# Kernel tuning notes

Measured on AMD Instinct MI355X. Metric: run time of the kernel, lower is better.

Reference implementation:

```python
import jax, jax.numpy as jnp
import numpy as np

N_NODES = 100000

def sage_conv(x, edge_index, Wl, bl, Wr):
    # PyG SAGEConv, aggr='add', normalize=False:
    #   out = lin_l(sum_{j in N(i)} x_j) + lin_r(x_i)
    src, dst = edge_index[0], edge_index[1]
    agg = jax.ops.segment_sum(x[src], dst, num_segments=N_NODES)  # [N, F]
    return agg @ Wl.T + bl + x @ Wr.T


def setup_inputs() -> dict:
    key = jax.random.key(0)
    ks = jax.random.split(key, 7)
    F_IN, HID, C, E = 128, 256, 50, 640000
    x = jax.random.normal(ks[0], (N_NODES, F_IN), dtype=jnp.float32)
    edge_index = jax.random.randint(ks[1], (2, E), 0, N_NODES, dtype=jnp.int64)
    s1 = 1.0 / np.sqrt(F_IN)
    s2 = 1.0 / np.sqrt(HID)
    return {
        "x": x,
        "edge_index": edge_index,
        "W1l": jax.random.normal(ks[2], (HID, F_IN), dtype=jnp.float32) * s1,
        "b1l": jnp.zeros((HID,), dtype=jnp.float32),
        "W1r": jax.random.normal(ks[3], (HID, F_IN), dtype=jnp.float32) * s1,
        "W2l": jax.random.normal(ks[4], (C, HID), dtype=jnp.float32) * s2,
        "b2l": jnp.zeros((C,), dtype=jnp.float32),
        "W2r": jax.random.normal(ks[5], (C, HID), dtype=jnp.float32) * s2,
    }


def reference(x, edge_index, W1l, b1l, W1r, W2l, b2l, W2r):
    h = sage_conv(x, edge_index, W1l, b1l, W1r)
    h = jax.nn.relu(h)
    # F.dropout(p=0.5, training=False) is identity in eval mode
    out = sage_conv(h, edge_index, W2l, b2l, W2r)
    return out
```

## Files before the change

kernel.cpp:

```cpp
#include <hip/hip_runtime.h>

#define N_NODES 100000
#define MPAD    100096
#define F_IN 128
#define HID 256
#define C_OUT 50
#define N_EDGES 640000
#define CAP 32
#define NRANGE 391
#define P1BLK 256
#define EPB (N_EDGES / P1BLK)
#define CCAP 32
#define XBLK 12500

typedef __attribute__((ext_vector_type(8))) short short8;
typedef __attribute__((ext_vector_type(8))) ushort us8;
typedef __attribute__((ext_vector_type(4))) float f32x4;

struct alignas(8) us4 { ushort x, y, z, w; };

__device__ __forceinline__ ushort f2bf(float f) {
    union { float f; unsigned u; } v; v.f = f;
    unsigned r = (v.u + 0x7fffu + ((v.u >> 16) & 1u)) >> 16;
    return (ushort)r;
}

__device__ __forceinline__ float bf2f(ushort u) {
    union { unsigned u; float f; } v; v.u = ((unsigned)u) << 16;
    return v.f;
}

__device__ __forceinline__ void load_lds16(const void* gsrc, void* lds) {
    __builtin_amdgcn_global_load_lds(
        (const __attribute__((address_space(1))) void*)gsrc,
        (__attribute__((address_space(3))) void*)lds, 16, 0, 0);
}

__global__ void prep_kernel(const float* __restrict__ W1l, const float* __restrict__ W1r,
                            const float* __restrict__ W2l, const float* __restrict__ W2r,
                            ushort* __restrict__ B1t, ushort* __restrict__ B2t) {
    int idx = blockIdx.x * blockDim.x + threadIdx.x;
    if (idx < 256 * 256) {
        int o = idx >> 8, k = idx & 255;
        float v = (k < 128) ? W1l[o * 128 + k] : W1r[o * 128 + (k - 128)];
        B1t[o * 256 + k] = f2bf(v);
    }
    if (idx < 128 * 256) {
        int c = idx >> 8, k = idx & 255;
        float v = 0.f;
        if (c < C_OUT) v = W2l[c * 256 + k];
        else if (c >= 64 && c < 64 + C_OUT) v = W2r[(c - 64) * 256 + k];
        B2t[c * 256 + k] = f2bf(v);
    }
}

__global__ __launch_bounds__(256) void phase1_xcvt(const int* __restrict__ src,
                                                   const int* __restrict__ dst,
                                                   int* __restrict__ cnt1,
                                                   int* __restrict__ subbucket,
                                                   const float* __restrict__ x,
                                                   ushort* __restrict__ A1) {
    __shared__ int lcnt[NRANGE];
    int b = blockIdx.x;
    if (b < P1BLK) {
        for (int r = threadIdx.x; r < NRANGE; r += 256) lcnt[r] = 0;
        __syncthreads();
        int base = b * EPB;
        for (int i = base + (int)threadIdx.x; i < base + EPB; i += 256) {
            int d = dst[i];
            int s = src[i];
            int r = d >> 8;
            int p = atomicAdd(&lcnt[r], 1);
            if (p < CCAP) subbucket[((size_t)r * P1BLK + b) * CCAP + p] = ((d & 255) << 24) | s;
        }
        __syncthreads();
        for (int r = threadIdx.x; r < NRANGE; r += 256) cnt1[r * P1BLK + b] = lcnt[r];
    } else {
        int tid = (b - P1BLK) * 256 + threadIdx.x;
        int node = tid >> 5, q = tid & 31;
        if (node >= N_NODES) return;
        float4 v = *reinterpret_cast<const float4*>(x + (size_t)node * F_IN + q * 4);
        us4 o;
        o.x = f2bf(v.x); o.y = f2bf(v.y); o.z = f2bf(v.z); o.w = f2bf(v.w);
        *reinterpret_cast<us4*>(&A1[(size_t)node * 256 + 128 + q * 4]) = o;
    }
}

__global__ __launch_bounds__(256) void phase2_merge(const int* __restrict__ cnt1,
                                                    const int* __restrict__ subbucket,
                                                    int* __restrict__ cnt,
                                                    int* __restrict__ bucket) {
    __shared__ int lcnt2[256];
    __shared__ int lbuf[256 * CAP];
    int r = blockIdx.x, t = threadIdx.x;
    lcnt2[t] = 0;
    __syncthreads();
    int n = cnt1[r * P1BLK + t];
    if (n > CCAP) n = CCAP;
    size_t cbase = ((size_t)r * P1BLK + t) * CCAP;
    for (int k = 0; k < n; ++k) {
        unsigned u = (unsigned)subbucket[cbase + k];
        int dl = u >> 24;
        int p = atomicAdd(&lcnt2[dl], 1);
        if (p < CAP) lbuf[dl * CAP + p] = (int)(u & 0xFFFFFF);
    }
    __syncthreads();
    int node0 = r << 8;
    if (node0 + t < N_NODES) cnt[node0 + t] = lcnt2[t];
    for (int idx = t; idx < 256 * CAP; idx += 256) {
        if (node0 + (idx >> 5) < N_NODES) bucket[(size_t)node0 * CAP + idx] = lbuf[idx];
    }
}

__global__ void gather1_kernel(const int* __restrict__ cnt, const int* __restrict__ bucket,
                               ushort* __restrict__ A1) {
    int tid = blockIdx.x * blockDim.x + threadIdx.x;
    int node = tid >> 4, q = tid & 15;
    if (node >= N_NODES) return;
    int n = cnt[node];
    if (n > CAP) n = CAP;
    const int* row = bucket + (size_t)node * CAP;
    float a[8];
#pragma unroll
    for (int j = 0; j < 8; ++j) a[j] = 0.f;
    int p = 0;
    while (p + 8 <= n) {
        us8 v[8];
#pragma unroll
        for (int t = 0; t < 8; ++t) {
            int s = row[p + t];
            v[t] = *reinterpret_cast<const us8*>(&A1[(size_t)s * 256 + 128 + q * 8]);
        }
#pragma unroll
        for (int t = 0; t < 8; ++t)
#pragma unroll
            for (int j = 0; j < 8; ++j) a[j] += bf2f(v[t][j]);
        p += 8;
    }
    int rem = n - p;
    if (rem > 0) {
        us8 v[7];
#pragma unroll
        for (int t = 0; t < 7; ++t) {
            int s = (t < rem) ? row[p + t] : row[p];
            v[t] = *reinterpret_cast<const us8*>(&A1[(size_t)s * 256 + 128 + q * 8]);
        }
#pragma unroll
        for (int t = 0; t < 7; ++t) {
            if (t < rem) {
#pragma unroll
                for (int j = 0; j < 8; ++j) a[j] += bf2f(v[t][j]);
            }
        }
    }
    us8 o;
#pragma unroll
    for (int j = 0; j < 8; ++j) o[j] = f2bf(a[j]);
    *reinterpret_cast<us8*>(&A1[(size_t)node * 256 + q * 8]) = o;
}

__global__ void gather2_kernel(const ushort* __restrict__ g, const int* __restrict__ cnt,
                               const int* __restrict__ bucket, float* __restrict__ out) {
    int tid = blockIdx.x * blockDim.x + threadIdx.x;
    int node = tid >> 3, q = tid & 7;
    if (node >= N_NODES) return;
    int c = q * 8;
    if (c >= C_OUT) return;
    int n = cnt[node];
    if (n > CAP) n = CAP;
    const int* row = bucket + (size_t)node * CAP;
    float a[8];
#pragma unroll
    for (int j = 0; j < 8; ++j) a[j] = 0.f;
    int p = 0;
    while (p + 8 <= n) {
        us8 v[8];
#pragma unroll
        for (int t = 0; t < 8; ++t) {
            int s = row[p + t];
            v[t] = *reinterpret_cast<const us8*>(&g[(size_t)s * 64 + c]);
        }
#pragma unroll
        for (int t = 0; t < 8; ++t)
#pragma unroll
            for (int j = 0; j < 8; ++j) a[j] += bf2f(v[t][j]);
        p += 8;
    }
    int rem = n - p;
    if (rem > 0) {
        us8 v[7];
#pragma unroll
        for (int t = 0; t < 7; ++t) {
            int s = (t < rem) ? row[p + t] : row[p];
            v[t] = *reinterpret_cast<const us8*>(&g[(size_t)s * 64 + c]);
        }
#pragma unroll
        for (int t = 0; t < 7; ++t) {
            if (t < rem) {
#pragma unroll
                for (int j = 0; j < 8; ++j) a[j] += bf2f(v[t][j]);
            }
        }
    }
    float* po = out + (size_t)node * C_OUT;
#pragma unroll
    for (int j = 0; j < 8; ++j) {
        if (c + j < C_OUT) po[c + j] += a[j];
    }
}

__global__ __launch_bounds__(512) void gemm_fused(
    const ushort* __restrict__ A, const ushort* __restrict__ B1,
    const ushort* __restrict__ B2, const float* __restrict__ b1,
    const float* __restrict__ b2, ushort* __restrict__ gOut,
    float* __restrict__ oOut) {
    __shared__ alignas(16) ushort smem[36864];
    ushort* As  = smem;
    ushort* Bs  = smem + 4096;
    ushort* hL  = smem;
    ushort* Bs2 = smem + 32768;

    const int tid = threadIdx.x;
    const int lane = tid & 63, wid = tid >> 6;
    const int wr = wid >> 2, wc = wid & 3;
    const int brow = blockIdx.x;
    const int aoffA = (lane & 15) * 32 + (lane >> 4) * 8;

    f32x4 acc[4][4];
#pragma unroll
    for (int m = 0; m < 4; ++m)
#pragma unroll
        for (int n = 0; n < 4; ++n) acc[m][n] = (f32x4){0.f, 0.f, 0.f, 0.f};

    const int rA = tid >> 2, kA = (tid & 3) * 8;
    const int cB1 = tid + 512;
    const int rB1 = cB1 >> 2, kB1 = (cB1 & 3) * 8;
    const size_t aRow = (size_t)(brow * 128 + rA) * 256;

    for (int kt = 0; kt < 8; ++kt) {
        const int kOff = kt * 32;
        load_lds16(A + aRow + kOff + kA, &As[tid * 8]);
        load_lds16(B1 + (size_t)rA * 256 + kOff + kA, &Bs[tid * 8]);
        load_lds16(B1 + (size_t)rB1 * 256 + kOff + kB1, &Bs[cB1 * 8]);
        __syncthreads();

        short8 af[4], bfr[4];
#pragma unroll
        for (int m = 0; m < 4; ++m)
            af[m] = *reinterpret_cast<const short8*>(&As[(wr * 64 + m * 16) * 32 + aoffA]);
#pragma unroll
        for (int n = 0; n < 4; ++n)
            bfr[n] = *reinterpret_cast<const short8*>(&Bs[(wc * 64 + n * 16) * 32 + aoffA]);
#pragma unroll
        for (int m = 0; m < 4; ++m)
#pragma unroll
            for (int n = 0; n < 4; ++n)
                acc[m][n] = __builtin_amdgcn_mfma_f32_16x16x32_bf16(af[m], bfr[n], acc[m][n], 0, 0, 0);
        __syncthreads();
    }

    {
        const int colBase = wc * 64 + (lane & 15);
        const int lrBase = wr * 64 + ((lane >> 4) << 2);
        float bv[4];
#pragma unroll
        for (int n = 0; n < 4; ++n) bv[n] = b1[colBase + n * 16];
#pragma unroll
        for (int m = 0; m < 4; ++m) {
#pragma unroll
            for (int r = 0; r < 4; ++r) {
                int lr = lrBase + m * 16 + r;
#pragma unroll
                for (int n = 0; n < 4; ++n) {
                    float v = acc[m][n][r] + bv[n];
                    v = v > 0.f ? v : 0.f;
                    int ktc = wc * 2 + (n >> 1);
                    int kp = (n & 1) * 16 + (lane & 15);
                    hL[ktc * 4096 + lr * 32 + kp] = f2bf(v);
                }
            }
        }
    }
    __syncthreads();

    f32x4 acc2[4][2];
#pragma unroll
    for (int m = 0; m < 4; ++m)
#pragma unroll
        for (int n = 0; n < 2; ++n) acc2[m][n] = (f32x4){0.f, 0.f, 0.f, 0.f};

    for (int kt = 0; kt < 8; ++kt) {
        const int kOff = kt * 32;
        load_lds16(B2 + (size_t)rA * 256 + kOff + kA, &Bs2[tid * 8]);
        __syncthreads();

        short8 af[4], bfr[2];
#pragma unroll
        for (int m = 0; m < 4; ++m)
            af[m] = *reinterpret_cast<const short8*>(&hL[kt * 4096 + (wr * 64 + m * 16) * 32 + aoffA]);
#pragma unroll
        for (int n = 0; n < 2; ++n)
            bfr[n] = *reinterpret_cast<const short8*>(&Bs2[(wc * 32 + n * 16) * 32 + aoffA]);
#pragma unroll
        for (int m = 0; m < 4; ++m)
#pragma unroll
            for (int n = 0; n < 2; ++n)
                acc2[m][n] = __builtin_amdgcn_mfma_f32_16x16x32_bf16(af[m], bfr[n], acc2[m][n], 0, 0, 0);
        __syncthreads();
    }

    const int colB = wc * 32 + (lane & 15);
    const int rowB = brow * 128 + wr * 64 + ((lane >> 4) << 2);
#pragma unroll
    for (int m = 0; m < 4; ++m) {
#pragma unroll
        for (int r = 0; r < 4; ++r) {
            int row = rowB + m * 16 + r;
            if (row >= N_NODES) continue;
#pragma unroll
            for (int n = 0; n < 2; ++n) {
                int cg = colB + n * 16;
                float v = acc2[m][n][r];
                if (cg < 64) {
                    gOut[(size_t)row * 64 + cg] = f2bf(v);
                } else if (cg < 64 + C_OUT) {
                    oOut[(size_t)row * C_OUT + (cg - 64)] = v + b2[cg - 64];
                }
            }
        }
    }
}

extern "C" void kernel_launch(void* const* d_in, const int* in_sizes, int n_in,
                              void* d_out, int out_size, void* d_ws, size_t ws_size,
                              hipStream_t stream) {
    const float* x   = (const float*)d_in[0];
    const int*   ei  = (const int*)d_in[1];
    const float* W1l = (const float*)d_in[2];
    const float* b1l = (const float*)d_in[3];
    const float* W1r = (const float*)d_in[4];
    const float* W2l = (const float*)d_in[5];
    const float* b2l = (const float*)d_in[6];
    const float* W2r = (const float*)d_in[7];
    float* out = (float*)d_out;

    ushort* A1    = (ushort*)d_ws;
    ushort* B1t   = A1 + (size_t)MPAD * 256;
    ushort* B2t   = B1t + 256 * 256;
    ushort* g     = B2t + 128 * 256;
    int* cnt      = (int*)(g + (size_t)N_NODES * 64);
    int* bucket   = cnt + N_NODES;
    int* cnt1     = bucket + (size_t)N_NODES * CAP;
    int* subbucket= cnt1 + NRANGE * P1BLK;

    const int* src = ei;
    const int* dst = ei + N_EDGES;

    prep_kernel<<<256, 256, 0, stream>>>(W1l, W1r, W2l, W2r, B1t, B2t);
    phase1_xcvt<<<P1BLK + XBLK, 256, 0, stream>>>(src, dst, cnt1, subbucket, x, A1);
    phase2_merge<<<NRANGE, 256, 0, stream>>>(cnt1, subbucket, cnt, bucket);

    gather1_kernel<<<(N_NODES * 16 + 255) / 256, 256, 0, stream>>>(cnt, bucket, A1);

    const int nbrow = MPAD / 128;
    gemm_fused<<<nbrow, 512, 0, stream>>>(A1, B1t, B2t, b1l, b2l, g, out);

    gather2_kernel<<<(N_NODES * 8 + 255) / 256, 256, 0, stream>>>(g, cnt, bucket, out);
}
```

Baseline: 165.8 us.

## Split fused two-layer GEMM into separate kernels with hidden buffer in global memory

The fused kernel kept the hidden ReLU activations in LDS and ran the second GEMM in the same block. It is now split into two kernels. The first writes bf16 hidden activations to a new global workspace buffer, and the second reads them back and produces both g and the output. The split frees LDS in the first kernel, which may allow higher occupancy, but it adds roughly 51MB of global write and read traffic plus an extra launch.

```diff
diff --git a/kernel.cpp b/kernel.cpp
--- a/kernel.cpp
+++ b/kernel.cpp
@@ -209,39 +209,34 @@
     }
 }
 
-__global__ __launch_bounds__(512) void gemm_fused(
-    const ushort* __restrict__ A, const ushort* __restrict__ B1,
-    const ushort* __restrict__ B2, const float* __restrict__ b1,
-    const float* __restrict__ b2, ushort* __restrict__ gOut,
-    float* __restrict__ oOut) {
-    __shared__ alignas(16) ushort smem[36864];
-    ushort* As  = smem;
-    ushort* Bs  = smem + 4096;
-    ushort* hL  = smem;
-    ushort* Bs2 = smem + 32768;
-
+__global__ __launch_bounds__(512) void gemm1_512(
+    const ushort* __restrict__ A, const ushort* __restrict__ B,
+    const float* __restrict__ bias, ushort* __restrict__ hOut) {
+    __shared__ alignas(16) ushort As[128 * 32];
+    __shared__ alignas(16) ushort Bs[256 * 32];
     const int tid = threadIdx.x;
     const int lane = tid & 63, wid = tid >> 6;
     const int wr = wid >> 2, wc = wid & 3;
     const int brow = blockIdx.x;
+
+    f32x4 acc[4][4];
+#pragma unroll
+    for (int m = 0; m < 4; ++m)
+#pragma unroll
+        for (int n = 0; n < 4; ++n) acc[m][n] = (f32x4){0.f, 0.f, 0.f, 0.f};
+
+    const int rA = tid >> 2,          kA = (tid & 3) * 8;
+    const int cB1 = tid + 512;
+    const int rB1 = cB1 >> 2,         kB1 = (cB1 & 3) * 8;
+    const size_t aRow = (size_t)(brow * 128 + rA) * 256;
+
     const int aoffA = (lane & 15) * 32 + (lane >> 4) * 8;
-
-    f32x4 acc[4][4];
-#pragma unroll
-    for (int m = 0; m < 4; ++m)
-#pragma unroll
-        for (int n = 0; n < 4; ++n) acc[m][n] = (f32x4){0.f, 0.f, 0.f, 0.f};
-
-    const int rA = tid >> 2, kA = (tid & 3) * 8;
-    const int cB1 = tid + 512;
-    const int rB1 = cB1 >> 2, kB1 = (cB1 & 3) * 8;
-    const size_t aRow = (size_t)(brow * 128 + rA) * 256;
 
     for (int kt = 0; kt < 8; ++kt) {
         const int kOff = kt * 32;
         load_lds16(A + aRow + kOff + kA, &As[tid * 8]);
-        load_lds16(B1 + (size_t)rA * 256 + kOff + kA, &Bs[tid * 8]);
-        load_lds16(B1 + (size_t)rB1 * 256 + kOff + kB1, &Bs[cB1 * 8]);
+        load_lds16(B + (size_t)rA * 256 + kOff + kA, &Bs[tid * 8]);
+        load_lds16(B + (size_t)rB1 * 256 + kOff + kB1, &Bs[cB1 * 8]);
         __syncthreads();
 
         short8 af[4], bfr[4];
@@ -259,58 +254,12 @@
         __syncthreads();
     }
 
-    {
-        const int colBase = wc * 64 + (lane & 15);
-        const int lrBase = wr * 64 + ((lane >> 4) << 2);
-        float bv[4];
-#pragma unroll
-        for (int n = 0; n < 4; ++n) bv[n] = b1[colBase + n * 16];
-#pragma unroll
-        for (int m = 0; m < 4; ++m) {
-#pragma unroll
-            for (int r = 0; r < 4; ++r) {
-                int lr = lrBase + m * 16 + r;
-#pragma unroll
-                for (int n = 0; n < 4; ++n) {
-                    float v = acc[m][n][r] + bv[n];
-                    v = v > 0.f ? v : 0.f;
-                    int ktc = wc * 2 + (n >> 1);
-                    int kp = (n & 1) * 16 + (lane & 15);
-                    hL[ktc * 4096 + lr * 32 + kp] = f2bf(v);
-                }
-            }
-        }
-    }
-    __syncthreads();
-
-    f32x4 acc2[4][2];
-#pragma unroll
-    for (int m = 0; m < 4; ++m)
-#pragma unroll
-        for (int n = 0; n < 2; ++n) acc2[m][n] = (f32x4){0.f, 0.f, 0.f, 0.f};
-
-    for (int kt = 0; kt < 8; ++kt) {
-        const int kOff = kt * 32;
-        load_lds16(B2 + (size_t)rA * 256 + kOff + kA, &Bs2[tid * 8]);
-        __syncthreads();
-
-        short8 af[4], bfr[2];
-#pragma unroll
-        for (int m = 0; m < 4; ++m)
-            af[m] = *reinterpret_cast<const short8*>(&hL[kt * 4096 + (wr * 64 + m * 16) * 32 + aoffA]);
-#pragma unroll
-        for (int n = 0; n < 2; ++n)
-            bfr[n] = *reinterpret_cast<const short8*>(&Bs2[(wc * 32 + n * 16) * 32 + aoffA]);
-#pragma unroll
-        for (int m = 0; m < 4; ++m)
-#pragma unroll
-            for (int n = 0; n < 2; ++n)
-                acc2[m][n] = __builtin_amdgcn_mfma_f32_16x16x32_bf16(af[m], bfr[n], acc2[m][n], 0, 0, 0);
-        __syncthreads();
-    }
-
-    const int colB = wc * 32 + (lane & 15);
+    const int colB = wc * 64 + (lane & 15);
     const int rowB = brow * 128 + wr * 64 + ((lane >> 4) << 2);
+
+    float bv[4];
+#pragma unroll
+    for (int n = 0; n < 4; ++n) bv[n] = bias[colB + n * 16];
 #pragma unroll
     for (int m = 0; m < 4; ++m) {
 #pragma unroll
@@ -318,13 +267,82 @@
             int row = rowB + m * 16 + r;
             if (row >= N_NODES) continue;
 #pragma unroll
-            for (int n = 0; n < 2; ++n) {
+            for (int n = 0; n < 4; ++n) {
+                float v = acc[m][n][r] + bv[n];
+                v = v > 0.f ? v : 0.f;
+                hOut[(size_t)row * 256 + colB + n * 16] = f2bf(v);
+            }
+        }
+    }
+}
+
+__global__ __launch_bounds__(256) void gemm2_kernel(
+    const ushort* __restrict__ A, const ushort* __restrict__ B,
+    const float* __restrict__ bias, ushort* __restrict__ gOut,
+    float* __restrict__ oOut) {
+    __shared__ alignas(16) ushort As[128 * 32];
+    __shared__ alignas(16) ushort Bs[128 * 32];
+    const int tid = threadIdx.x;
+    const int lane = tid & 63, wid = tid >> 6;
+    const int wr = wid >> 1, wc = wid & 1;
+    const int brow = blockIdx.x;
+
+    f32x4 acc[4][4];
+#pragma unroll
+    for (int m = 0; m < 4; ++m)
+#pragma unroll
+        for (int n = 0; n < 4; ++n) acc[m][n] = (f32x4){0.f, 0.f, 0.f, 0.f};
+
+    const int c0 = tid, c1 = tid + 256;
+    const int r0 = c0 >> 2, k80 = (c0 & 3) * 8;
+    const int r1 = c1 >> 2, k81 = (c1 & 3) * 8;
+    const size_t aRow0 = (size_t)(brow * 128 + r0) * 256;
+    const size_t aRow1 = (size_t)(brow * 128 + r1) * 256;
+    const size_t bRow0 = (size_t)r0 * 256;
+    const size_t bRow1 = (size_t)r1 * 256;
+
+    const int aoffA = (lane & 15) * 32 + (lane >> 4) * 8;
+
+    for (int kt = 0; kt < 8; ++kt) {
+        const int kOff = kt * 32;
+        load_lds16(A + aRow0 + kOff + k80, &As[c0 * 8]);
+        load_lds16(A + aRow1 + kOff + k81, &As[c1 * 8]);
+        load_lds16(B + bRow0 + kOff + k80, &Bs[c0 * 8]);
+        load_lds16(B + bRow1 + kOff + k81, &Bs[c1 * 8]);
+        __syncthreads();
+
+        short8 af[4], bfr[4];
+#pragma unroll
+        for (int m = 0; m < 4; ++m)
+            af[m] = *reinterpret_cast<const short8*>(&As[(wr * 64 + m * 16) * 32 + aoffA]);
+#pragma unroll
+        for (int n = 0; n < 4; ++n)
+            bfr[n] = *reinterpret_cast<const short8*>(&Bs[(wc * 64 + n * 16) * 32 + aoffA]);
+#pragma unroll
+        for (int m = 0; m < 4; ++m)
+#pragma unroll
+            for (int n = 0; n < 4; ++n)
+                acc[m][n] = __builtin_amdgcn_mfma_f32_16x16x32_bf16(af[m], bfr[n], acc[m][n], 0, 0, 0);
+        __syncthreads();
+    }
+
+    const int colB = wc * 64 + (lane & 15);
+    const int rowB = brow * 128 + wr * 64 + ((lane >> 4) << 2);
+
+#pragma unroll
+    for (int m = 0; m < 4; ++m) {
+#pragma unroll
+        for (int r = 0; r < 4; ++r) {
+            int row = rowB + m * 16 + r;
+            if (row >= N_NODES) continue;
+#pragma unroll
+            for (int n = 0; n < 4; ++n) {
                 int cg = colB + n * 16;
-                float v = acc2[m][n][r];
+                float v = acc[m][n][r];
                 if (cg < 64) {
                     gOut[(size_t)row * 64 + cg] = f2bf(v);
                 } else if (cg < 64 + C_OUT) {
-                    oOut[(size_t)row * C_OUT + (cg - 64)] = v + b2[cg - 64];
+                    oOut[(size_t)row * C_OUT + (cg - 64)] = v + bias[cg - 64];
                 }
             }
         }
@@ -345,7 +363,8 @@
     float* out = (float*)d_out;
 
     ushort* A1    = (ushort*)d_ws;
-    ushort* B1t   = A1 + (size_t)MPAD * 256;
+    ushort* hbuf  = A1 + (size_t)MPAD * 256;
+    ushort* B1t   = hbuf + (size_t)MPAD * 256;
     ushort* B2t   = B1t + 256 * 256;
     ushort* g     = B2t + 128 * 256;
     int* cnt      = (int*)(g + (size_t)N_NODES * 64);
@@ -363,7 +382,8 @@
     gather1_kernel<<<(N_NODES * 16 + 255) / 256, 256, 0, stream>>>(cnt, bucket, A1);
 
     const int nbrow = MPAD / 128;
-    gemm_fused<<<nbrow, 512, 0, stream>>>(A1, B1t, B2t, b1l, b2l, g, out);
+    gemm1_512<<<nbrow, 512, 0, stream>>>(A1, B1t, b1l, hbuf);
+    gemm2_kernel<<<nbrow, 256, 0, stream>>>(hbuf, B2t, b2l, g, out);
 
     gather2_kernel<<<(N_NODES * 8 + 255) / 256, 256, 0, stream>>>(g, cnt, bucket, out);
 }
```

Measured after the change: 152.1 us. 8.2% less time.
